# Optimization experiments

Measured on AMD Instinct MI355X. Metric: run time of the kernel, lower is better.

## Reference

```python
import jax, jax.numpy as jnp
import numpy as np
import math

B, H, N, D = 8, 8, 2048, 64
CLIP = 10.0
NEG_INF = 1.0e10

def setup_inputs() -> dict:
    key = jax.random.key(0)
    kq, kk, kv, km = jax.random.split(key, 4)
    Q = jax.random.normal(kq, (B, H, N, D), dtype=jnp.float32)
    K = jax.random.normal(kk, (B, H, N, D), dtype=jnp.float32)
    V = jax.random.normal(kv, (B, H, N, D), dtype=jnp.float32)
    mask = jax.random.randint(km, (B, N, 1), 0, 2).astype(jnp.bool_)
    return {"Q": Q, "K": K, "V": V, "mask": mask}

def reference(Q, K, V, mask):
    scale = math.sqrt(Q.shape[-1])
    # logits: (B, H, Nq, Nk)
    logits = jnp.einsum("bhqd,bhkd->bhqk", Q, K) / scale
    logits = CLIP * jnp.tanh(logits)
    # mask (B, N, 1) -> broadcast over heads and query dim along key axis
    m = mask[:, None, None, :, 0]  # (B, 1, 1, Nk)
    logits = jnp.where(m, -NEG_INF, logits)
    probs = jax.nn.softmax(logits, axis=-1)
    return jnp.einsum("bhqk,bhkd->bhqd", probs, V)
```

## Files before the change

### kernel.cpp

```cpp
#include <hip/hip_runtime.h>

typedef __attribute__((ext_vector_type(8))) short short8;
typedef __attribute__((ext_vector_type(8))) _Float16 half8;
typedef __attribute__((ext_vector_type(16))) float f32x16;
typedef __attribute__((ext_vector_type(4))) float f32x4;
typedef __attribute__((ext_vector_type(4))) unsigned short u16x4;
typedef __attribute__((ext_vector_type(8))) unsigned short u16x8;
typedef unsigned int u32;
typedef unsigned short u16;

#define B_ 8
#define H_ 8
#define N_ 2048
#define D_ 64
#define PSTR 72
#define ELEMS 8388608
#define WS_NEED (3ull * 16777216ull + 65536ull + 4096ull)

static __device__ inline u16 bfhi(float x) {
  u32 u = __float_as_uint(x);
  return (u16)((u + 0x7FFFu + ((u >> 16) & 1u)) >> 16);
}
static __device__ inline float bf2f(u16 h) { return __uint_as_float((u32)h << 16); }
static __device__ inline u16 h2u(_Float16 h) { union { _Float16 f; u16 u; } c; c.f = h; return c.u; }

__global__ __launch_bounds__(256) void mask_scan(
    const int* __restrict__ maskg, int* __restrict__ idx, int* __restrict__ cnt) {
  const int b = blockIdx.x, tid = threadIdx.x;
  __shared__ int sc[256];
  const int n0 = tid * 8;
  u32 bits = 0;
  int c = 0;
#pragma unroll
  for (int i = 0; i < 8; ++i) {
    if (maskg[b * N_ + n0 + i] == 0) { bits |= (1u << i); ++c; }
  }
  sc[tid] = c;
  __syncthreads();
  for (int off = 1; off < 256; off <<= 1) {
    int v = (tid >= off) ? sc[tid - off] : 0;
    __syncthreads();
    sc[tid] += v;
    __syncthreads();
  }
  const int total = sc[255];
  int o = sc[tid] - c;
#pragma unroll
  for (int i = 0; i < 8; ++i)
    if (bits & (1u << i)) idx[b * N_ + (o++)] = n0 + i;
  if (tid < 64) {
    int j = total + tid;
    if (j < ((total + 63) & ~63)) idx[b * N_ + j] = -1;
  }
  if (tid == 0) cnt[b] = total;
}

__global__ __launch_bounds__(256) void conv_kv2(
    const float* __restrict__ K, const float* __restrict__ V,
    const int* __restrict__ idx, const int* __restrict__ cnt,
    u16* __restrict__ Khi, u16* __restrict__ Klo, u16* __restrict__ VThi) {
  const int kt = blockIdx.x, bh = blockIdx.y, b = bh >> 3, tid = threadIdx.x;
  const int cntb = cnt[b];
  const int nt = (cntb + 63) >> 6;
  if (kt >= nt) return;
  __shared__ float sT[64 * 68];
  __shared__ int sIdx[64];
  if (tid < 64) sIdx[tid] = idx[b * N_ + kt * 64 + tid];
  __syncthreads();
  const size_t ibh = (size_t)bh * N_ * D_;
  const size_t okb = ibh + (size_t)kt * 64 * D_;
#pragma unroll
  for (int cc = 0; cc < 2; ++cc) {
    const int c = tid + cc * 256, row = c >> 3, seg = c & 7;
    const int n = sIdx[row];
    f32x4 a, b2, va, vb;
    if (n >= 0) {
      const float* kp = K + ibh + (size_t)n * D_ + seg * 8;
      a  = *(const f32x4*)kp;
      b2 = *(const f32x4*)(kp + 4);
      const float* vp = V + ibh + (size_t)n * D_ + seg * 8;
      va = *(const f32x4*)vp;
      vb = *(const f32x4*)(vp + 4);
    } else {
#pragma unroll
      for (int j = 0; j < 4; ++j) { a[j] = 0.f; b2[j] = 0.f; va[j] = 0.f; vb[j] = 0.f; }
    }
    u16x8 h, l;
#pragma unroll
    for (int j = 0; j < 4; ++j) {
      _Float16 h0 = (_Float16)a[j];
      h[j] = h2u(h0); l[j] = h2u((_Float16)(a[j] - (float)h0));
      _Float16 h1 = (_Float16)b2[j];
      h[j + 4] = h2u(h1); l[j + 4] = h2u((_Float16)(b2[j] - (float)h1));
    }
    *(u16x8*)&Khi[okb + row * D_ + seg * 8] = h;
    *(u16x8*)&Klo[okb + row * D_ + seg * 8] = l;
    *(f32x4*)&sT[row * 68 + seg * 8]     = va;
    *(f32x4*)&sT[row * 68 + seg * 8 + 4] = vb;
  }
  __syncthreads();
  const int d = tid >> 2, ks = tid & 3;
  u16x8 h0, h1;
#pragma unroll
  for (int i = 0; i < 8; ++i) {
    h0[i] = h2u((_Float16)sT[(ks * 16 + i) * 68 + d]);
    h1[i] = h2u((_Float16)sT[(ks * 16 + i + 8) * 68 + d]);
  }
  const size_t ob = (size_t)bh * D_ * N_ + (size_t)d * N_ + (size_t)kt * 64 + ks * 16;
  *(u16x8*)&VThi[ob] = h0; *(u16x8*)&VThi[ob + 8] = h1;
}

__global__ __launch_bounds__(256, 4) void attn_mfma3(
    const float* __restrict__ Qg,
    const u16* __restrict__ Khi, const u16* __restrict__ Klo,
    const u16* __restrict__ VThi,
    const int* __restrict__ cnt, float* __restrict__ Og)
{
  const int qtile = blockIdx.x;
  const int bh = blockIdx.y, b = bh >> 3;
  const int tid = threadIdx.x, w = tid >> 6, lane = tid & 63;
  const int l32 = lane & 31, hl = lane >> 5;
  const int cntb = cnt[b];
  const int nt = (cntb + 63) >> 6;

  __shared__ short sKbuf[2 * 64 * PSTR];
  __shared__ short sVh[64 * PSTR];
  __shared__ float sM[64];
  short* const sKh = sKbuf;
  short* const sKl = sKbuf + 64 * PSTR;
  short* const sP  = sKbuf;

  half8 qfh[4], qfl[4];
  {
    const float* qp = Qg + ((size_t)bh * N_ + qtile * 128 + w * 32 + l32) * D_ + hl * 8;
#pragma unroll
    for (int s = 0; s < 4; ++s) {
      f32x4 a = *(const f32x4*)(qp + s * 16);
      f32x4 c = *(const f32x4*)(qp + s * 16 + 4);
#pragma unroll
      for (int j = 0; j < 4; ++j) {
        _Float16 h0 = (_Float16)a[j];
        qfh[s][j] = h0; qfl[s][j] = (_Float16)(a[j] - (float)h0);
        _Float16 h1 = (_Float16)c[j];
        qfh[s][j + 4] = h1; qfl[s][j + 4] = (_Float16)(c[j] - (float)h1);
      }
    }
  }
  half8 ones;
#pragma unroll
  for (int j = 0; j < 8; ++j) ones[j] = (l32 == 0) ? (_Float16)1.f : (_Float16)0.f;

  f32x16 accO0, accO1, accD;
#pragma unroll
  for (int i = 0; i < 16; ++i) { accO0[i] = 0.f; accO1[i] = 0.f; accD[i] = 0.f; }

  const size_t kvb = (size_t)bh * N_ * D_;

  for (int kt = 0; kt < nt; ++kt) {
    const int k0 = kt * 64;
    __syncthreads();

#pragma unroll
    for (int cc = 0; cc < 2; ++cc) {
      const int c = tid + cc * 256, row = c >> 3, seg = c & 7;
      const int lofs = row * PSTR + seg * 8;
      const size_t kofs = kvb + (size_t)(k0 + row) * D_ + seg * 8;
      *(short8*)&sKh[lofs] = *(const short8*)&Khi[kofs];
      *(short8*)&sKl[lofs] = *(const short8*)&Klo[kofs];
      const size_t vofs = kvb + (size_t)row * N_ + k0 + seg * 8;
      *(short8*)&sVh[lofs] = *(const short8*)&VThi[vofs];
    }
    if (tid < 64) sM[tid] = (k0 + tid < cntb) ? 0.f : -16384.f;
    __syncthreads();

    f32x16 S0, S1;
#pragma unroll
    for (int i = 0; i < 16; ++i) { S0[i] = 0.f; S1[i] = 0.f; }
    __builtin_amdgcn_s_setprio(1);
#pragma unroll
    for (int s = 0; s < 4; ++s) {
      const int o0 = l32 * PSTR + s * 16 + hl * 8;
      half8 kfh = *(const half8*)&sKh[o0];
      half8 kfl = *(const half8*)&sKl[o0];
      S0 = __builtin_amdgcn_mfma_f32_32x32x16_f16(qfh[s], kfh, S0, 0, 0, 0);
      S0 = __builtin_amdgcn_mfma_f32_32x32x16_f16(qfl[s], kfh, S0, 0, 0, 0);
      S0 = __builtin_amdgcn_mfma_f32_32x32x16_f16(qfh[s], kfl, S0, 0, 0, 0);
      const int o1 = (32 + l32) * PSTR + s * 16 + hl * 8;
      half8 kgh = *(const half8*)&sKh[o1];
      half8 kgl = *(const half8*)&sKl[o1];
      S1 = __builtin_amdgcn_mfma_f32_32x32x16_f16(qfh[s], kgh, S1, 0, 0, 0);
      S1 = __builtin_amdgcn_mfma_f32_32x32x16_f16(qfl[s], kgh, S1, 0, 0, 0);
      S1 = __builtin_amdgcn_mfma_f32_32x32x16_f16(qfh[s], kgl, S1, 0, 0, 0);
    }
    __builtin_amdgcn_s_setprio(0);
    __syncthreads();

    const float bias0 = sM[l32], bias1 = sM[32 + l32];
#pragma unroll
    for (int r = 0; r < 16; ++r) {
      const int row = w * 32 + (r & 3) + 8 * (r >> 2) + 4 * hl;
      {
        float s  = S0[r];
        float z  = __builtin_amdgcn_exp2f(fabsf(s) * -0.36067376022224087f);
        float nu = (s >= 0.f) ? z : 1.f;
        float e  = __builtin_fmaf(nu * __builtin_amdgcn_rcpf(1.f + z),
                                  -28.853900817779268f, bias0);
        float p  = __builtin_amdgcn_exp2f(e);
        sP[row * PSTR + l32] = (short)h2u((_Float16)p);
      }
      {
        float s  = S1[r];
        float z  = __builtin_amdgcn_exp2f(fabsf(s) * -0.36067376022224087f);
        float nu = (s >= 0.f) ? z : 1.f;
        float e  = __builtin_fmaf(nu * __builtin_amdgcn_rcpf(1.f + z),
                                  -28.853900817779268f, bias1);
        float p  = __builtin_amdgcn_exp2f(e);
        sP[row * PSTR + 32 + l32] = (short)h2u((_Float16)p);
      }
    }
    __syncthreads();

    __builtin_amdgcn_s_setprio(1);
#pragma unroll
    for (int s = 0; s < 4; ++s) {
      half8 pf = *(const half8*)&sP[(w * 32 + l32) * PSTR + s * 16 + hl * 8];
      const int o0 = l32 * PSTR + s * 16 + hl * 8;
      half8 v0 = *(const half8*)&sVh[o0];
      accO0 = __builtin_amdgcn_mfma_f32_32x32x16_f16(pf, v0, accO0, 0, 0, 0);
      const int o1 = (32 + l32) * PSTR + s * 16 + hl * 8;
      half8 v1 = *(const half8*)&sVh[o1];
      accO1 = __builtin_amdgcn_mfma_f32_32x32x16_f16(pf, v1, accO1, 0, 0, 0);
      accD  = __builtin_amdgcn_mfma_f32_32x32x16_f16(pf, ones, accD, 0, 0, 0);
    }
    __builtin_amdgcn_s_setprio(0);
  }

  const size_t obase = (size_t)bh * N_ + qtile * 128 + w * 32;
#pragma unroll
  for (int r = 0; r < 16; ++r) {
    float den = __shfl(accD[r], lane & 32);
    float inv = (den > 0.f) ? (1.f / den) : 0.f;
    const int row = (r & 3) + 8 * (r >> 2) + 4 * hl;
    Og[(obase + row) * D_ + l32]      = accO0[r] * inv;
    Og[(obase + row) * D_ + 32 + l32] = accO1[r] * inv;
  }
}

__global__ __launch_bounds__(256, 3) void attn_mfma(
    const float* __restrict__ Qg, const float* __restrict__ Kg,
    const float* __restrict__ Vg, const int* __restrict__ maskg,
    float* __restrict__ Og)
{
  const int qtile = blockIdx.x;
  const int bh    = blockIdx.y;
  const int b     = bh >> 3;
  const int tid   = threadIdx.x;
  const int w     = tid >> 6;
  const int lane  = tid & 63;
  const int l32   = lane & 31;
  const int hl    = lane >> 5;
  const int qh    = w >> 1;
  const int kh    = w & 1;

  __shared__ short sKh[64 * PSTR], sKl[64 * PSTR];
  __shared__ short sVh[64 * PSTR], sVl[64 * PSTR];
  __shared__ short sP [64 * PSTR];
  __shared__ float sM[64];

  short8 qfh[4], qfl[4];
  {
    const float* qp = Qg + ((size_t)bh * N_ + qtile * 64 + qh * 32 + l32) * D_ + hl * 8;
#pragma unroll
    for (int s = 0; s < 4; ++s) {
      f32x4 a = *(const f32x4*)(qp + s * 16);
      f32x4 c = *(const f32x4*)(qp + s * 16 + 4);
#pragma unroll
      for (int j = 0; j < 4; ++j) {
        u16 h0 = bfhi(a[j]);
        qfh[s][j] = (short)h0;
        qfl[s][j] = (short)bfhi(a[j] - bf2f(h0));
        u16 h1 = bfhi(c[j]);
        qfh[s][j + 4] = (short)h1;
        qfl[s][j + 4] = (short)bfhi(c[j] - bf2f(h1));
      }
    }
  }
  short8 ones;
#pragma unroll
  for (int j = 0; j < 8; ++j) ones[j] = (short)((l32 == 0) ? 0x3F80 : 0);
  f32x16 accO, accD;
#pragma unroll
  for (int i = 0; i < 16; ++i) { accO[i] = 0.f; accD[i] = 0.f; }
  const size_t kvbase = (size_t)bh * N_ * D_;

  for (int kt = 0; kt < N_ / 64; ++kt) {
    const int k0 = kt * 64;
    __syncthreads();
    {
      const int row = tid >> 2, seg = tid & 3;
      const float* kp = Kg + kvbase + (size_t)(k0 + row) * D_ + seg * 16;
      short8 h0, h1, l0, l1;
#pragma unroll
      for (int i2 = 0; i2 < 2; ++i2) {
        f32x4 t0 = *(const f32x4*)(kp + i2 * 8);
        f32x4 t1 = *(const f32x4*)(kp + i2 * 8 + 4);
#pragma unroll
        for (int j = 0; j < 4; ++j) {
          u16 ha = bfhi(t0[j]); u16 la = bfhi(t0[j] - bf2f(ha));
          u16 hb = bfhi(t1[j]); u16 lb = bfhi(t1[j] - bf2f(hb));
          if (i2 == 0) { h0[j]=(short)ha; l0[j]=(short)la; h0[j+4]=(short)hb; l0[j+4]=(short)lb; }
          else         { h1[j]=(short)ha; l1[j]=(short)la; h1[j+4]=(short)hb; l1[j+4]=(short)lb; }
        }
      }
      *(short8*)&sKh[row * PSTR + seg * 16]     = h0;
      *(short8*)&sKh[row * PSTR + seg * 16 + 8] = h1;
      *(short8*)&sKl[row * PSTR + seg * 16]     = l0;
      *(short8*)&sKl[row * PSTR + seg * 16 + 8] = l1;
    }
    {
      const float* vp = Vg + kvbase + (size_t)(k0 + w * 16) * D_ + lane;
      float vv[16];
#pragma unroll
      for (int kk = 0; kk < 16; ++kk) vv[kk] = vp[(size_t)kk * D_];
      short8 h0, h1, l0, l1;
#pragma unroll
      for (int kk = 0; kk < 8; ++kk) {
        u16 ha = bfhi(vv[kk]);     h0[kk]=(short)ha; l0[kk]=(short)bfhi(vv[kk]-bf2f(ha));
        u16 hb = bfhi(vv[kk + 8]); h1[kk]=(short)hb; l1[kk]=(short)bfhi(vv[kk+8]-bf2f(hb));
      }
      *(short8*)&sVh[lane * PSTR + w * 16]     = h0;
      *(short8*)&sVh[lane * PSTR + w * 16 + 8] = h1;
      *(short8*)&sVl[lane * PSTR + w * 16]     = l0;
      *(short8*)&sVl[lane * PSTR + w * 16 + 8] = l1;
    }
    if (tid < 64) sM[tid] = maskg[b * N_ + k0 + tid] ? 0.f : 1.f;
    __syncthreads();

    f32x16 S;
#pragma unroll
    for (int i = 0; i < 16; ++i) S[i] = 0.f;
#pragma unroll
    for (int s = 0; s < 4; ++s) {
      const int off = (kh * 32 + l32) * PSTR + s * 16 + hl * 8;
      short8 kfh = *(const short8*)&sKh[off];
      short8 kfl = *(const short8*)&sKl[off];
      S = __builtin_amdgcn_mfma_f32_32x32x16_bf16(qfh[s], kfh, S, 0, 0, 0);
      S = __builtin_amdgcn_mfma_f32_32x32x16_bf16(qfl[s], kfh, S, 0, 0, 0);
      S = __builtin_amdgcn_mfma_f32_32x32x16_bf16(qfh[s], kfl, S, 0, 0, 0);
    }
    const float pm = sM[kh * 32 + l32];
#pragma unroll
    for (int r = 0; r < 16; ++r) {
      float x  = S[r] * 0.125f;
      float ax = fminf(fabsf(x), 30.f);
      float z  = __builtin_amdgcn_exp2f(ax * -2.8853900817779268f);
      float nu = (x >= 0.f) ? z : 1.f;
      float e  = nu * __builtin_amdgcn_rcpf(1.f + z) * -28.853900817779268f;
      float p  = __builtin_amdgcn_exp2f(e) * pm;
      const int row = qh * 32 + (r & 3) + 8 * (r >> 2) + 4 * hl;
      sP[row * PSTR + kh * 32 + l32] = (short)bfhi(p);
    }
    __syncthreads();
#pragma unroll
    for (int s = 0; s < 4; ++s) {
      short8 pf  = *(const short8*)&sP[(qh * 32 + l32) * PSTR + s * 16 + hl * 8];
      const int voff = (kh * 32 + l32) * PSTR + s * 16 + hl * 8;
      short8 vfh = *(const short8*)&sVh[voff];
      short8 vfl = *(const short8*)&sVl[voff];
      accO = __builtin_amdgcn_mfma_f32_32x32x16_bf16(pf, vfh, accO, 0, 0, 0);
      accO = __builtin_amdgcn_mfma_f32_32x32x16_bf16(pf, vfl, accO, 0, 0, 0);
      accD = __builtin_amdgcn_mfma_f32_32x32x16_bf16(pf, ones, accD, 0, 0, 0);
    }
  }
  const size_t obase = (size_t)bh * N_ + qtile * 64 + qh * 32;
#pragma unroll
  for (int r = 0; r < 16; ++r) {
    float den = __shfl(accD[r], lane & 32);
    float inv = (den > 0.f) ? (1.f / den) : 0.f;
    const int row = (r & 3) + 8 * (r >> 2) + 4 * hl;
    Og[(obase + row) * D_ + kh * 32 + l32] = accO[r] * inv;
  }
}

extern "C" void kernel_launch(void* const* d_in, const int* in_sizes, int n_in,
                              void* d_out, int out_size, void* d_ws, size_t ws_size,
                              hipStream_t stream) {
  const float* Q = (const float*)d_in[0];
  const float* K = (const float*)d_in[1];
  const float* V = (const float*)d_in[2];
  const int* mask = (const int*)d_in[3];
  float* out = (float*)d_out;
  dim3 block(256);
  if (ws_size >= (size_t)WS_NEED) {
    u16* wsp  = (u16*)d_ws;
    u16* Khi  = wsp;
    u16* Klo  = wsp + ELEMS;
    u16* VThi = wsp + 2 * (size_t)ELEMS;
    int* idxp = (int*)(wsp + 3 * (size_t)ELEMS);
    int* cntp = idxp + 8 * N_;
    mask_scan<<<dim3(8), block, 0, stream>>>(mask, idxp, cntp);
    conv_kv2<<<dim3(32, 64), block, 0, stream>>>(K, V, idxp, cntp, Khi, Klo, VThi);
    attn_mfma3<<<dim3(16, 64), block, 0, stream>>>(Q, Khi, Klo, VThi, cntp, out);
  } else {
    attn_mfma<<<dim3(32, 64), block, 0, stream>>>(Q, K, V, mask, out);
  }
}
```

Measured before the change: 268.4 us.

## Double-buffer K tiles via direct global-to-LDS loads with pre-swizzled tiled workspace

The conversion kernel now writes K (hi/lo) and transposed V into per-tile contiguous blocks with an XOR swizzle baked in. The attention kernel uses global_load_lds to copy these tiles straight into LDS, prefetching the next K tile into a second buffer while the current one is being processed. Waits are done with manual vmcnt/lgkmcnt counters and raw barriers. This is meant to hide global latency and remove register staging and LDS bank conflicts. In exchange, correctness depends on hand-counted waitcnt values, and P now reuses the current K buffer.

```diff
diff --git a/kernel.cpp b/kernel.cpp
--- a/kernel.cpp
+++ b/kernel.cpp
@@ -4,7 +4,6 @@
 typedef __attribute__((ext_vector_type(8))) _Float16 half8;
 typedef __attribute__((ext_vector_type(16))) float f32x16;
 typedef __attribute__((ext_vector_type(4))) float f32x4;
-typedef __attribute__((ext_vector_type(4))) unsigned short u16x4;
 typedef __attribute__((ext_vector_type(8))) unsigned short u16x8;
 typedef unsigned int u32;
 typedef unsigned short u16;
@@ -14,8 +13,10 @@
 #define N_ 2048
 #define D_ 64
 #define PSTR 72
-#define ELEMS 8388608
-#define WS_NEED (3ull * 16777216ull + 65536ull + 4096ull)
+#define NTILE_MAX 32
+#define KWS_SHORTS 16777216ull
+#define VWS_SHORTS 8388608ull
+#define WS_NEED ((48ull << 20) + 131072ull)
 
 static __device__ inline u16 bfhi(float x) {
   u32 u = __float_as_uint(x);
@@ -23,6 +24,12 @@
 }
 static __device__ inline float bf2f(u16 h) { return __uint_as_float((u32)h << 16); }
 static __device__ inline u16 h2u(_Float16 h) { union { _Float16 f; u16 u; } c; c.f = h; return c.u; }
+
+static __device__ __forceinline__ void gload16(const void* g, void* l) {
+  __builtin_amdgcn_global_load_lds(
+      (const __attribute__((address_space(1))) void*)g,
+      (__attribute__((address_space(3))) void*)l, 16, 0, 0);
+}
 
 __global__ __launch_bounds__(256) void mask_scan(
     const int* __restrict__ maskg, int* __restrict__ idx, int* __restrict__ cnt) {
@@ -58,32 +65,30 @@
 __global__ __launch_bounds__(256) void conv_kv2(
     const float* __restrict__ K, const float* __restrict__ V,
     const int* __restrict__ idx, const int* __restrict__ cnt,
-    u16* __restrict__ Khi, u16* __restrict__ Klo, u16* __restrict__ VThi) {
+    u16* __restrict__ Kws, u16* __restrict__ Vws) {
   const int kt = blockIdx.x, bh = blockIdx.y, b = bh >> 3, tid = threadIdx.x;
   const int cntb = cnt[b];
   const int nt = (cntb + 63) >> 6;
   if (kt >= nt) return;
   __shared__ float sT[64 * 68];
-  __shared__ int sIdx[64];
-  if (tid < 64) sIdx[tid] = idx[b * N_ + kt * 64 + tid];
-  __syncthreads();
   const size_t ibh = (size_t)bh * N_ * D_;
-  const size_t okb = ibh + (size_t)kt * 64 * D_;
+  u16* const kb = Kws + ((size_t)bh * NTILE_MAX + kt) * 8192;
+  u16* const vb = Vws + ((size_t)bh * NTILE_MAX + kt) * 4096;
 #pragma unroll
   for (int cc = 0; cc < 2; ++cc) {
     const int c = tid + cc * 256, row = c >> 3, seg = c & 7;
-    const int n = sIdx[row];
-    f32x4 a, b2, va, vb;
+    const int n = idx[b * N_ + kt * 64 + row];
+    f32x4 a, b2, va, vb2;
     if (n >= 0) {
       const float* kp = K + ibh + (size_t)n * D_ + seg * 8;
       a  = *(const f32x4*)kp;
       b2 = *(const f32x4*)(kp + 4);
       const float* vp = V + ibh + (size_t)n * D_ + seg * 8;
-      va = *(const f32x4*)vp;
-      vb = *(const f32x4*)(vp + 4);
+      va  = *(const f32x4*)vp;
+      vb2 = *(const f32x4*)(vp + 4);
     } else {
 #pragma unroll
-      for (int j = 0; j < 4; ++j) { a[j] = 0.f; b2[j] = 0.f; va[j] = 0.f; vb[j] = 0.f; }
+      for (int j = 0; j < 4; ++j) { a[j] = 0.f; b2[j] = 0.f; va[j] = 0.f; vb2[j] = 0.f; }
     }
     u16x8 h, l;
 #pragma unroll
@@ -93,10 +98,11 @@
       _Float16 h1 = (_Float16)b2[j];
       h[j + 4] = h2u(h1); l[j + 4] = h2u((_Float16)(b2[j] - (float)h1));
     }
-    *(u16x8*)&Khi[okb + row * D_ + seg * 8] = h;
-    *(u16x8*)&Klo[okb + row * D_ + seg * 8] = l;
+    const int ps = seg ^ (row & 7);
+    *(u16x8*)&kb[row * 64 + ps * 8] = h;
+    *(u16x8*)&kb[4096 + row * 64 + ps * 8] = l;
     *(f32x4*)&sT[row * 68 + seg * 8]     = va;
-    *(f32x4*)&sT[row * 68 + seg * 8 + 4] = vb;
+    *(f32x4*)&sT[row * 68 + seg * 8 + 4] = vb2;
   }
   __syncthreads();
   const int d = tid >> 2, ks = tid & 3;
@@ -106,14 +112,14 @@
     h0[i] = h2u((_Float16)sT[(ks * 16 + i) * 68 + d]);
     h1[i] = h2u((_Float16)sT[(ks * 16 + i + 8) * 68 + d]);
   }
-  const size_t ob = (size_t)bh * D_ * N_ + (size_t)d * N_ + (size_t)kt * 64 + ks * 16;
-  *(u16x8*)&VThi[ob] = h0; *(u16x8*)&VThi[ob + 8] = h1;
-}
-
-__global__ __launch_bounds__(256, 4) void attn_mfma3(
+  const int p0 = (2 * ks) ^ (d & 7), p1 = (2 * ks + 1) ^ (d & 7);
+  *(u16x8*)&vb[d * 64 + p0 * 8] = h0;
+  *(u16x8*)&vb[d * 64 + p1 * 8] = h1;
+}
+
+__global__ __launch_bounds__(256, 4) void attn_mfma4(
     const float* __restrict__ Qg,
-    const u16* __restrict__ Khi, const u16* __restrict__ Klo,
-    const u16* __restrict__ VThi,
+    const u16* __restrict__ Kws, const u16* __restrict__ Vws,
     const int* __restrict__ cnt, float* __restrict__ Og)
 {
   const int qtile = blockIdx.x;
@@ -123,12 +129,10 @@
   const int cntb = cnt[b];
   const int nt = (cntb + 63) >> 6;
 
-  __shared__ short sKbuf[2 * 64 * PSTR];
-  __shared__ short sVh[64 * PSTR];
-  __shared__ float sM[64];
-  short* const sKh = sKbuf;
-  short* const sKl = sKbuf + 64 * PSTR;
-  short* const sP  = sKbuf;
+  __shared__ __align__(16) char sMem[40960];
+  char* const sK0 = sMem;
+  char* const sK1 = sMem + 16384;
+  char* const sV  = sMem + 32768;
 
   half8 qfh[4], qfl[4];
   {
@@ -154,24 +158,30 @@
 #pragma unroll
   for (int i = 0; i < 16; ++i) { accO0[i] = 0.f; accO1[i] = 0.f; accD[i] = 0.f; }
 
-  const size_t kvb = (size_t)bh * N_ * D_;
+  const char* const kbase = (const char*)(Kws + (size_t)bh * NTILE_MAX * 8192);
+  const char* const vbase = (const char*)(Vws + (size_t)bh * NTILE_MAX * 4096);
+  const int xr = l32 & 7;
+  const int stg = w * 1024 + (lane << 4);
+
+  asm volatile("s_waitcnt vmcnt(0) lgkmcnt(0)" ::: "memory");
+#pragma unroll
+  for (int i = 0; i < 4; ++i)
+    gload16(kbase + i * 4096 + stg, sK0 + i * 4096 + w * 1024);
 
   for (int kt = 0; kt < nt; ++kt) {
-    const int k0 = kt * 64;
-    __syncthreads();
-
-#pragma unroll
-    for (int cc = 0; cc < 2; ++cc) {
-      const int c = tid + cc * 256, row = c >> 3, seg = c & 7;
-      const int lofs = row * PSTR + seg * 8;
-      const size_t kofs = kvb + (size_t)(k0 + row) * D_ + seg * 8;
-      *(short8*)&sKh[lofs] = *(const short8*)&Khi[kofs];
-      *(short8*)&sKl[lofs] = *(const short8*)&Klo[kofs];
-      const size_t vofs = kvb + (size_t)row * N_ + k0 + seg * 8;
-      *(short8*)&sVh[lofs] = *(const short8*)&VThi[vofs];
-    }
-    if (tid < 64) sM[tid] = (k0 + tid < cntb) ? 0.f : -16384.f;
-    __syncthreads();
+    char* const sKc = (kt & 1) ? sK1 : sK0;
+    char* const sKn = (kt & 1) ? sK0 : sK1;
+    const int ktn = (kt + 1 < nt) ? kt + 1 : nt - 1;
+
+#pragma unroll
+    for (int i = 0; i < 2; ++i)
+      gload16(vbase + (size_t)kt * 8192 + i * 4096 + stg, sV + i * 4096 + w * 1024);
+#pragma unroll
+    for (int i = 0; i < 4; ++i)
+      gload16(kbase + (size_t)ktn * 16384 + i * 4096 + stg, sKn + i * 4096 + w * 1024);
+
+    asm volatile("s_waitcnt vmcnt(6)" ::: "memory");
+    __builtin_amdgcn_s_barrier();
 
     f32x16 S0, S1;
 #pragma unroll
@@ -179,26 +189,31 @@
     __builtin_amdgcn_s_setprio(1);
 #pragma unroll
     for (int s = 0; s < 4; ++s) {
-      const int o0 = l32 * PSTR + s * 16 + hl * 8;
-      half8 kfh = *(const half8*)&sKh[o0];
-      half8 kfl = *(const half8*)&sKl[o0];
+      const int sl = ((2 * s + hl) ^ xr) << 4;
+      const int o0 = l32 * 128 + sl;
+      half8 kfh = *(const half8*)(sKc + o0);
+      half8 kfl = *(const half8*)(sKc + 8192 + o0);
       S0 = __builtin_amdgcn_mfma_f32_32x32x16_f16(qfh[s], kfh, S0, 0, 0, 0);
       S0 = __builtin_amdgcn_mfma_f32_32x32x16_f16(qfl[s], kfh, S0, 0, 0, 0);
       S0 = __builtin_amdgcn_mfma_f32_32x32x16_f16(qfh[s], kfl, S0, 0, 0, 0);
-      const int o1 = (32 + l32) * PSTR + s * 16 + hl * 8;
-      half8 kgh = *(const half8*)&sKh[o1];
-      half8 kgl = *(const half8*)&sKl[o1];
+      const int o1 = (32 + l32) * 128 + sl;
+      half8 kgh = *(const half8*)(sKc + o1);
+      half8 kgl = *(const half8*)(sKc + 8192 + o1);
       S1 = __builtin_amdgcn_mfma_f32_32x32x16_f16(qfh[s], kgh, S1, 0, 0, 0);
       S1 = __builtin_amdgcn_mfma_f32_32x32x16_f16(qfl[s], kgh, S1, 0, 0, 0);
       S1 = __builtin_amdgcn_mfma_f32_32x32x16_f16(qfh[s], kgl, S1, 0, 0, 0);
     }
     __builtin_amdgcn_s_setprio(0);
-    __syncthreads();
-
-    const float bias0 = sM[l32], bias1 = sM[32 + l32];
+    asm volatile("s_waitcnt lgkmcnt(0)" ::: "memory");
+    __builtin_amdgcn_s_barrier();
+
+    const float bias0 = (kt * 64 + l32      < cntb) ? 0.f : -16384.f;
+    const float bias1 = (kt * 64 + 32 + l32 < cntb) ? 0.f : -16384.f;
+    const int pco = ((2 * l32) & 15);
 #pragma unroll
     for (int r = 0; r < 16; ++r) {
-      const int row = w * 32 + (r & 3) + 8 * (r >> 2) + 4 * hl;
+      const int prow = w * 32 + (r & 3) + 8 * (r >> 2) + 4 * hl;
+      const int pr7 = prow & 7;
       {
         float s  = S0[r];
         float z  = __builtin_amdgcn_exp2f(fabsf(s) * -0.36067376022224087f);
@@ -206,7 +221,7 @@
         float e  = __builtin_fmaf(nu * __builtin_amdgcn_rcpf(1.f + z),
                                   -28.853900817779268f, bias0);
         float p  = __builtin_amdgcn_exp2f(e);
-        sP[row * PSTR + l32] = (short)h2u((_Float16)p);
+        *(short*)(sKc + prow * 128 + (((l32 >> 3) ^ pr7) << 4) + pco) = (short)h2u((_Float16)p);
       }
       {
         float s  = S1[r];
@@ -215,24 +230,26 @@
         float e  = __builtin_fmaf(nu * __builtin_amdgcn_rcpf(1.f + z),
                                   -28.853900817779268f, bias1);
         float p  = __builtin_amdgcn_exp2f(e);
-        sP[row * PSTR + 32 + l32] = (short)h2u((_Float16)p);
-      }
-    }
-    __syncthreads();
+        *(short*)(sKc + prow * 128 + ((((l32 >> 3) + 4) ^ pr7) << 4) + pco) = (short)h2u((_Float16)p);
+      }
+    }
+    asm volatile("s_waitcnt lgkmcnt(0) vmcnt(4)" ::: "memory");
+    __builtin_amdgcn_s_barrier();
 
     __builtin_amdgcn_s_setprio(1);
 #pragma unroll
     for (int s = 0; s < 4; ++s) {
-      half8 pf = *(const half8*)&sP[(w * 32 + l32) * PSTR + s * 16 + hl * 8];
-      const int o0 = l32 * PSTR + s * 16 + hl * 8;
-      half8 v0 = *(const half8*)&sVh[o0];
+      const int sl = ((2 * s + hl) ^ xr) << 4;
+      half8 pf = *(const half8*)(sKc + (w * 32 + l32) * 128 + sl);
+      half8 v0 = *(const half8*)(sV + l32 * 128 + sl);
       accO0 = __builtin_amdgcn_mfma_f32_32x32x16_f16(pf, v0, accO0, 0, 0, 0);
-      const int o1 = (32 + l32) * PSTR + s * 16 + hl * 8;
-      half8 v1 = *(const half8*)&sVh[o1];
+      half8 v1 = *(const half8*)(sV + (32 + l32) * 128 + sl);
       accO1 = __builtin_amdgcn_mfma_f32_32x32x16_f16(pf, v1, accO1, 0, 0, 0);
       accD  = __builtin_amdgcn_mfma_f32_32x32x16_f16(pf, ones, accD, 0, 0, 0);
     }
     __builtin_amdgcn_s_setprio(0);
+    asm volatile("s_waitcnt lgkmcnt(0)" ::: "memory");
+    __builtin_amdgcn_s_barrier();
   }
 
   const size_t obase = (size_t)bh * N_ + qtile * 128 + w * 32;
@@ -393,14 +410,13 @@
   dim3 block(256);
   if (ws_size >= (size_t)WS_NEED) {
     u16* wsp  = (u16*)d_ws;
-    u16* Khi  = wsp;
-    u16* Klo  = wsp + ELEMS;
-    u16* VThi = wsp + 2 * (size_t)ELEMS;
-    int* idxp = (int*)(wsp + 3 * (size_t)ELEMS);
+    u16* Kws  = wsp;
+    u16* Vws  = wsp + KWS_SHORTS;
+    int* idxp = (int*)(wsp + KWS_SHORTS + VWS_SHORTS);
     int* cntp = idxp + 8 * N_;
     mask_scan<<<dim3(8), block, 0, stream>>>(mask, idxp, cntp);
-    conv_kv2<<<dim3(32, 64), block, 0, stream>>>(K, V, idxp, cntp, Khi, Klo, VThi);
-    attn_mfma3<<<dim3(16, 64), block, 0, stream>>>(Q, Khi, Klo, VThi, cntp, out);
+    conv_kv2<<<dim3(32, 64), block, 0, stream>>>(K, V, idxp, cntp, Kws, Vws);
+    attn_mfma4<<<dim3(16, 64), block, 0, stream>>>(Q, Kws, Vws, cntp, out);
   } else {
     attn_mfma<<<dim3(32, 64), block, 0, stream>>>(Q, K, V, mask, out);
   }
```

Result: slower. 385.0 us (+43.4%).

## Keep softmax probabilities in registers via transposed QK and permlane swap; fuse mask scan

Applied to the files above, without the earlier changes.

The QK MFMA operands are swapped so S comes out transposed, letting each lane pack its probabilities into f16 A-operand fragments with cvt_pkrtz and permlane32_swap. This removes the LDS round-trip for P and two barriers per key tile. The mask bias array is replaced by a tail-only branch on the last partial tile. Separately, the mask compaction scan is folded into conv_kv2, with each block recomputing the prefix scan through wave shuffles, so one kernel launch disappears. The costs are redundant scan work in every conversion block and extra register pressure from holding the packed P fragments.

```diff
diff --git a/kernel.cpp b/kernel.cpp
--- a/kernel.cpp
+++ b/kernel.cpp
@@ -2,9 +2,10 @@
 
 typedef __attribute__((ext_vector_type(8))) short short8;
 typedef __attribute__((ext_vector_type(8))) _Float16 half8;
+typedef __attribute__((ext_vector_type(2))) __fp16 fp16x2;
+typedef __attribute__((ext_vector_type(2))) unsigned int uint2v;
 typedef __attribute__((ext_vector_type(16))) float f32x16;
 typedef __attribute__((ext_vector_type(4))) float f32x4;
-typedef __attribute__((ext_vector_type(4))) unsigned short u16x4;
 typedef __attribute__((ext_vector_type(8))) unsigned short u16x8;
 typedef unsigned int u32;
 typedef unsigned short u16;
@@ -15,7 +16,7 @@
 #define D_ 64
 #define PSTR 72
 #define ELEMS 8388608
-#define WS_NEED (3ull * 16777216ull + 65536ull + 4096ull)
+#define WS_NEED ((48ull << 20) + 4096ull)
 
 static __device__ inline u16 bfhi(float x) {
   u32 u = __float_as_uint(x);
@@ -24,66 +25,111 @@
 static __device__ inline float bf2f(u16 h) { return __uint_as_float((u32)h << 16); }
 static __device__ inline u16 h2u(_Float16 h) { union { _Float16 f; u16 u; } c; c.f = h; return c.u; }
 
-__global__ __launch_bounds__(256) void mask_scan(
-    const int* __restrict__ maskg, int* __restrict__ idx, int* __restrict__ cnt) {
-  const int b = blockIdx.x, tid = threadIdx.x;
-  __shared__ int sc[256];
-  const int n0 = tid * 8;
-  u32 bits = 0;
-  int c = 0;
-#pragma unroll
-  for (int i = 0; i < 8; ++i) {
-    if (maskg[b * N_ + n0 + i] == 0) { bits |= (1u << i); ++c; }
-  }
-  sc[tid] = c;
-  __syncthreads();
-  for (int off = 1; off < 256; off <<= 1) {
-    int v = (tid >= off) ? sc[tid - off] : 0;
-    __syncthreads();
-    sc[tid] += v;
-    __syncthreads();
-  }
-  const int total = sc[255];
-  int o = sc[tid] - c;
-#pragma unroll
-  for (int i = 0; i < 8; ++i)
-    if (bits & (1u << i)) idx[b * N_ + (o++)] = n0 + i;
-  if (tid < 64) {
-    int j = total + tid;
-    if (j < ((total + 63) & ~63)) idx[b * N_ + j] = -1;
-  }
-  if (tid == 0) cnt[b] = total;
+static __device__ __forceinline__ u32 pkrtz_u32(float a, float b) {
+  union { fp16x2 h; u32 u; } c;
+  c.h = __builtin_amdgcn_cvt_pkrtz(a, b);
+  return c.u;
+}
+
+template <bool TAIL>
+static __device__ __forceinline__ void softmax_repack(
+    const f32x16& S0, const f32x16& S1, int rem, half8 pa[4]) {
+  float p0[16], p1[16];
+#pragma unroll
+  for (int r = 0; r < 16; ++r) {
+    const int kap = (r & 3) + 8 * (r >> 2);
+    {
+      float s  = S0[r];
+      float z  = __builtin_amdgcn_exp2f(fabsf(s) * -0.36067376022224087f);
+      float nu = (s >= 0.f) ? z : 1.f;
+      float e  = nu * __builtin_amdgcn_rcpf(1.f + z) * -28.853900817779268f;
+      if (TAIL) e = (kap < rem) ? e : -16384.f;
+      p0[r] = __builtin_amdgcn_exp2f(e);
+    }
+    {
+      float s  = S1[r];
+      float z  = __builtin_amdgcn_exp2f(fabsf(s) * -0.36067376022224087f);
+      float nu = (s >= 0.f) ? z : 1.f;
+      float e  = nu * __builtin_amdgcn_rcpf(1.f + z) * -28.853900817779268f;
+      if (TAIL) e = (kap + 32 < rem) ? e : -16384.f;
+      p1[r] = __builtin_amdgcn_exp2f(e);
+    }
+  }
+#pragma unroll
+  for (int h = 0; h < 2; ++h) {
+    const float* p = h ? p1 : p0;
+#pragma unroll
+    for (int g = 0; g < 2; ++g) {
+      u32 E0 = pkrtz_u32(p[8 * g + 0], p[8 * g + 1]);
+      u32 E1 = pkrtz_u32(p[8 * g + 2], p[8 * g + 3]);
+      u32 O0 = pkrtz_u32(p[8 * g + 4], p[8 * g + 5]);
+      u32 O1 = pkrtz_u32(p[8 * g + 6], p[8 * g + 7]);
+      uint2v w0 = __builtin_amdgcn_permlane32_swap(E0, O0, false, false);
+      uint2v w1 = __builtin_amdgcn_permlane32_swap(E1, O1, false, false);
+      union { u32 u[4]; half8 v; } c;
+      c.u[0] = w0[0]; c.u[1] = w1[0]; c.u[2] = w0[1]; c.u[3] = w1[1];
+      pa[2 * h + g] = c.v;
+    }
+  }
 }
 
 __global__ __launch_bounds__(256) void conv_kv2(
     const float* __restrict__ K, const float* __restrict__ V,
-    const int* __restrict__ idx, const int* __restrict__ cnt,
-    u16* __restrict__ Khi, u16* __restrict__ Klo, u16* __restrict__ VThi) {
+    const int* __restrict__ maskg,
+    u16* __restrict__ Khi, u16* __restrict__ Klo, u16* __restrict__ VThi,
+    int* __restrict__ cnt) {
   const int kt = blockIdx.x, bh = blockIdx.y, b = bh >> 3, tid = threadIdx.x;
-  const int cntb = cnt[b];
+  const int lane = tid & 63, wv = tid >> 6;
+  __shared__ float sT[64 * 68];
+  __shared__ int sIdx[64];
+  __shared__ int wsum[4];
+  const int n0 = tid * 8;
+  u32 bits = 0; int c = 0;
+#pragma unroll
+  for (int i = 0; i < 8; ++i)
+    if (maskg[b * N_ + n0 + i] == 0) { bits |= (1u << i); ++c; }
+  int inc = c;
+#pragma unroll
+  for (int off = 1; off < 64; off <<= 1) {
+    int v = __shfl_up(inc, off);
+    if (lane >= off) inc += v;
+  }
+  if (lane == 63) wsum[wv] = inc;
+  if (tid < 64) sIdx[tid] = -1;
+  __syncthreads();
+  const int cntb = wsum[0] + wsum[1] + wsum[2] + wsum[3];
+  int o = inc - c;
+#pragma unroll
+  for (int k2 = 0; k2 < 4; ++k2) if (k2 < wv) o += wsum[k2];
+  const int k0 = kt * 64;
+#pragma unroll
+  for (int i = 0; i < 8; ++i)
+    if (bits & (1u << i)) {
+      if (o >= k0 && o < k0 + 64) sIdx[o - k0] = n0 + i;
+      ++o;
+    }
+  if (kt == 0 && (bh & 7) == 0 && tid == 0) cnt[b] = cntb;
+  __syncthreads();
   const int nt = (cntb + 63) >> 6;
   if (kt >= nt) return;
-  __shared__ float sT[64 * 68];
-  __shared__ int sIdx[64];
-  if (tid < 64) sIdx[tid] = idx[b * N_ + kt * 64 + tid];
-  __syncthreads();
+
   const size_t ibh = (size_t)bh * N_ * D_;
   const size_t okb = ibh + (size_t)kt * 64 * D_;
 #pragma unroll
   for (int cc = 0; cc < 2; ++cc) {
-    const int c = tid + cc * 256, row = c >> 3, seg = c & 7;
+    const int ci = tid + cc * 256, row = ci >> 3, seg = ci & 7;
     const int n = sIdx[row];
-    f32x4 a, b2, va, vb;
+    f32x4 a, b2, va, vb2;
     if (n >= 0) {
       const float* kp = K + ibh + (size_t)n * D_ + seg * 8;
       a  = *(const f32x4*)kp;
       b2 = *(const f32x4*)(kp + 4);
       const float* vp = V + ibh + (size_t)n * D_ + seg * 8;
-      va = *(const f32x4*)vp;
-      vb = *(const f32x4*)(vp + 4);
+      va  = *(const f32x4*)vp;
+      vb2 = *(const f32x4*)(vp + 4);
     } else {
 #pragma unroll
-      for (int j = 0; j < 4; ++j) { a[j] = 0.f; b2[j] = 0.f; va[j] = 0.f; vb[j] = 0.f; }
+      for (int j = 0; j < 4; ++j) { a[j] = 0.f; b2[j] = 0.f; va[j] = 0.f; vb2[j] = 0.f; }
     }
     u16x8 h, l;
 #pragma unroll
@@ -96,7 +142,7 @@
     *(u16x8*)&Khi[okb + row * D_ + seg * 8] = h;
     *(u16x8*)&Klo[okb + row * D_ + seg * 8] = l;
     *(f32x4*)&sT[row * 68 + seg * 8]     = va;
-    *(f32x4*)&sT[row * 68 + seg * 8 + 4] = vb;
+    *(f32x4*)&sT[row * 68 + seg * 8 + 4] = vb2;
   }
   __syncthreads();
   const int d = tid >> 2, ks = tid & 3;
@@ -110,7 +156,7 @@
   *(u16x8*)&VThi[ob] = h0; *(u16x8*)&VThi[ob + 8] = h1;
 }
 
-__global__ __launch_bounds__(256, 4) void attn_mfma3(
+__global__ __launch_bounds__(256, 4) void attn_mfma5(
     const float* __restrict__ Qg,
     const u16* __restrict__ Khi, const u16* __restrict__ Klo,
     const u16* __restrict__ VThi,
@@ -122,13 +168,10 @@
   const int l32 = lane & 31, hl = lane >> 5;
   const int cntb = cnt[b];
   const int nt = (cntb + 63) >> 6;
-
-  __shared__ short sKbuf[2 * 64 * PSTR];
+  const bool partial = (cntb & 63) != 0;
+
+  __shared__ short sKh[64 * PSTR], sKl[64 * PSTR];
   __shared__ short sVh[64 * PSTR];
-  __shared__ float sM[64];
-  short* const sKh = sKbuf;
-  short* const sKl = sKbuf + 64 * PSTR;
-  short* const sP  = sKbuf;
 
   half8 qfh[4], qfl[4];
   {
@@ -162,7 +205,7 @@
 
 #pragma unroll
     for (int cc = 0; cc < 2; ++cc) {
-      const int c = tid + cc * 256, row = c >> 3, seg = c & 7;
+      const int ci = tid + cc * 256, row = ci >> 3, seg = ci & 7;
       const int lofs = row * PSTR + seg * 8;
       const size_t kofs = kvb + (size_t)(k0 + row) * D_ + seg * 8;
       *(short8*)&sKh[lofs] = *(const short8*)&Khi[kofs];
@@ -170,7 +213,6 @@
       const size_t vofs = kvb + (size_t)row * N_ + k0 + seg * 8;
       *(short8*)&sVh[lofs] = *(const short8*)&VThi[vofs];
     }
-    if (tid < 64) sM[tid] = (k0 + tid < cntb) ? 0.f : -16384.f;
     __syncthreads();
 
     f32x16 S0, S1;
@@ -182,55 +224,34 @@
       const int o0 = l32 * PSTR + s * 16 + hl * 8;
       half8 kfh = *(const half8*)&sKh[o0];
       half8 kfl = *(const half8*)&sKl[o0];
-      S0 = __builtin_amdgcn_mfma_f32_32x32x16_f16(qfh[s], kfh, S0, 0, 0, 0);
-      S0 = __builtin_amdgcn_mfma_f32_32x32x16_f16(qfl[s], kfh, S0, 0, 0, 0);
-      S0 = __builtin_amdgcn_mfma_f32_32x32x16_f16(qfh[s], kfl, S0, 0, 0, 0);
+      S0 = __builtin_amdgcn_mfma_f32_32x32x16_f16(kfh, qfh[s], S0, 0, 0, 0);
+      S0 = __builtin_amdgcn_mfma_f32_32x32x16_f16(kfl, qfh[s], S0, 0, 0, 0);
+      S0 = __builtin_amdgcn_mfma_f32_32x32x16_f16(kfh, qfl[s], S0, 0, 0, 0);
       const int o1 = (32 + l32) * PSTR + s * 16 + hl * 8;
       half8 kgh = *(const half8*)&sKh[o1];
       half8 kgl = *(const half8*)&sKl[o1];
-      S1 = __builtin_amdgcn_mfma_f32_32x32x16_f16(qfh[s], kgh, S1, 0, 0, 0);
-      S1 = __builtin_amdgcn_mfma_f32_32x32x16_f16(qfl[s], kgh, S1, 0, 0, 0);
-      S1 = __builtin_amdgcn_mfma_f32_32x32x16_f16(qfh[s], kgl, S1, 0, 0, 0);
+      S1 = __builtin_amdgcn_mfma_f32_32x32x16_f16(kgh, qfh[s], S1, 0, 0, 0);
+      S1 = __builtin_amdgcn_mfma_f32_32x32x16_f16(kgl, qfh[s], S1, 0, 0, 0);
+      S1 = __builtin_amdgcn_mfma_f32_32x32x16_f16(kgh, qfl[s], S1, 0, 0, 0);
     }
     __builtin_amdgcn_s_setprio(0);
-    __syncthreads();
-
-    const float bias0 = sM[l32], bias1 = sM[32 + l32];
-#pragma unroll
-    for (int r = 0; r < 16; ++r) {
-      const int row = w * 32 + (r & 3) + 8 * (r >> 2) + 4 * hl;
-      {
-        float s  = S0[r];
-        float z  = __builtin_amdgcn_exp2f(fabsf(s) * -0.36067376022224087f);
-        float nu = (s >= 0.f) ? z : 1.f;
-        float e  = __builtin_fmaf(nu * __builtin_amdgcn_rcpf(1.f + z),
-                                  -28.853900817779268f, bias0);
-        float p  = __builtin_amdgcn_exp2f(e);
-        sP[row * PSTR + l32] = (short)h2u((_Float16)p);
-      }
-      {
-        float s  = S1[r];
-        float z  = __builtin_amdgcn_exp2f(fabsf(s) * -0.36067376022224087f);
-        float nu = (s >= 0.f) ? z : 1.f;
-        float e  = __builtin_fmaf(nu * __builtin_amdgcn_rcpf(1.f + z),
-                                  -28.853900817779268f, bias1);
-        float p  = __builtin_amdgcn_exp2f(e);
-        sP[row * PSTR + 32 + l32] = (short)h2u((_Float16)p);
-      }
-    }
-    __syncthreads();
+
+    half8 pa[4];
+    if (partial && kt == nt - 1)
+      softmax_repack<true>(S0, S1, cntb - k0 - 4 * hl, pa);
+    else
+      softmax_repack<false>(S0, S1, 0, pa);
 
     __builtin_amdgcn_s_setprio(1);
 #pragma unroll
     for (int s = 0; s < 4; ++s) {
-      half8 pf = *(const half8*)&sP[(w * 32 + l32) * PSTR + s * 16 + hl * 8];
       const int o0 = l32 * PSTR + s * 16 + hl * 8;
       half8 v0 = *(const half8*)&sVh[o0];
-      accO0 = __builtin_amdgcn_mfma_f32_32x32x16_f16(pf, v0, accO0, 0, 0, 0);
+      accO0 = __builtin_amdgcn_mfma_f32_32x32x16_f16(pa[s], v0, accO0, 0, 0, 0);
       const int o1 = (32 + l32) * PSTR + s * 16 + hl * 8;
       half8 v1 = *(const half8*)&sVh[o1];
-      accO1 = __builtin_amdgcn_mfma_f32_32x32x16_f16(pf, v1, accO1, 0, 0, 0);
-      accD  = __builtin_amdgcn_mfma_f32_32x32x16_f16(pf, ones, accD, 0, 0, 0);
+      accO1 = __builtin_amdgcn_mfma_f32_32x32x16_f16(pa[s], v1, accO1, 0, 0, 0);
+      accD  = __builtin_amdgcn_mfma_f32_32x32x16_f16(pa[s], ones, accD, 0, 0, 0);
     }
     __builtin_amdgcn_s_setprio(0);
   }
@@ -396,11 +417,9 @@
     u16* Khi  = wsp;
     u16* Klo  = wsp + ELEMS;
     u16* VThi = wsp + 2 * (size_t)ELEMS;
-    int* idxp = (int*)(wsp + 3 * (size_t)ELEMS);
-    int* cntp = idxp + 8 * N_;
-    mask_scan<<<dim3(8), block, 0, stream>>>(mask, idxp, cntp);
-    conv_kv2<<<dim3(32, 64), block, 0, stream>>>(K, V, idxp, cntp, Khi, Klo, VThi);
-    attn_mfma3<<<dim3(16, 64), block, 0, stream>>>(Q, Khi, Klo, VThi, cntp, out);
+    int* cntp = (int*)(wsp + 3 * (size_t)ELEMS);
+    conv_kv2<<<dim3(32, 64), block, 0, stream>>>(K, V, mask, Khi, Klo, VThi, cntp);
+    attn_mfma5<<<dim3(16, 64), block, 0, stream>>>(Q, Khi, Klo, VThi, cntp, out);
   } else {
     attn_mfma<<<dim3(32, 64), block, 0, stream>>>(Q, K, V, mask, out);
   }
```

New measurement: 382.2 us. 42.4% more time.
